# Kernel optimization log

Hardware: AMD Instinct MI355X
Metric: run time of the kernel (lower is better)

The kernel has to match this reference:

```python
import jax, jax.numpy as jnp
import numpy as np

EPSILON = 1e-05


def setup_inputs() -> dict:
    key = jax.random.key(0)
    X = jax.random.normal(key, (4, 2048, 3), dtype=jnp.float32)
    K = jnp.ones((), dtype=jnp.float32)
    B = jnp.zeros((), dtype=jnp.float32)
    return {"X": X, "K": K, "B": B}


def reference(X, K, B):
    # X: [batch, N, D]
    delta_X = X[:, :, None, :] - X[:, None, :, :]          # [b, N, N, D]
    sq = jnp.sum(delta_X * delta_X, axis=-1, keepdims=True)  # [b, N, N, 1]
    # safe sqrt: distance is 0 on the diagonal; avoid nan-producing grad paths
    distance = jnp.sqrt(jnp.where(sq == 0, 1.0, sq))
    distance = jnp.where(sq == 0, 0.0, distance)
    direction = delta_X / (distance + EPSILON)
    force = (K * (distance - B)) * direction               # [b, N, N, D]
    aggregated_force = jnp.sum(force, axis=-2)             # [b, N, D]
    return X + aggregated_force
```

## Files before the change

kernel.cpp:

```cpp
#include <hip/hip_runtime.h>

#define NPTS 2048

__global__ __launch_bounds__(256, 4) void spring_kernel(
    const float* __restrict__ X,
    const float* __restrict__ Kp,
    const float* __restrict__ Bp,
    float* __restrict__ out)
{
    __shared__ __align__(16) float xs[NPTS];
    __shared__ __align__(16) float ys[NPTS];
    __shared__ __align__(16) float zs[NPTS];

    const int tid    = threadIdx.x;
    const int b      = blockIdx.x >> 8;
    const int i_base = (blockIdx.x & 255) << 3;
    const float* Xb  = X + b * (NPTS * 3);

    const float K  = Kp[0];
    const float KB = K * Bp[0];

    {
        const float4* Xb4 = (const float4*)Xb;
        float4* xs4w = (float4*)xs;
        float4* ys4w = (float4*)ys;
        float4* zs4w = (float4*)zs;
        #pragma unroll
        for (int g0 = 0; g0 < NPTS / 4; g0 += 256) {
            const int g = g0 + tid;
            float4 f0 = Xb4[3 * g + 0];
            float4 f1 = Xb4[3 * g + 1];
            float4 f2 = Xb4[3 * g + 2];
            xs4w[g] = make_float4(f0.x, f0.w, f1.z, f2.y);
            ys4w[g] = make_float4(f0.y, f1.x, f1.w, f2.z);
            zs4w[g] = make_float4(f0.z, f1.y, f2.x, f2.w);
        }
    }
    __syncthreads();

    const int wv   = tid >> 6;
    const int lane = tid & 63;
    const int i0   = i_base + wv * 2;

    const float xi0 = xs[i0],     yi0 = ys[i0],     zi0 = zs[i0];
    const float xi1 = xs[i0 + 1], yi1 = ys[i0 + 1], zi1 = zs[i0 + 1];

    float ax0 = 0.f, ay0 = 0.f, az0 = 0.f;
    float ax1 = 0.f, ay1 = 0.f, az1 = 0.f;

    const float4* xs4 = (const float4*)xs;
    const float4* ys4 = (const float4*)ys;
    const float4* zs4 = (const float4*)zs;

    #pragma unroll 4
    for (int t = 0; t < NPTS / 4 / 64; ++t) {
        const int idx = (t << 6) + lane;
        float4 jx = xs4[idx];
        float4 jy = ys4[idx];
        float4 jz = zs4[idx];
        const float jxa[4] = {jx.x, jx.y, jx.z, jx.w};
        const float jya[4] = {jy.x, jy.y, jy.z, jy.w};
        const float jza[4] = {jz.x, jz.y, jz.z, jz.w};

        #pragma unroll
        for (int c = 0; c < 4; ++c) {
            {
                float dx = xi0 - jxa[c];
                float dy = yi0 - jya[c];
                float dz = zi0 - jza[c];
                float sq = fmaf(dx, dx, fmaf(dy, dy, fmaf(dz, dz, 1e-30f)));
                float r  = __builtin_amdgcn_rsqf(sq);
                float s  = fmaf(-KB, r, K);
                ax0 = fmaf(dx, s, ax0);
                ay0 = fmaf(dy, s, ay0);
                az0 = fmaf(dz, s, az0);
            }
            {
                float dx = xi1 - jxa[c];
                float dy = yi1 - jya[c];
                float dz = zi1 - jza[c];
                float sq = fmaf(dx, dx, fmaf(dy, dy, fmaf(dz, dz, 1e-30f)));
                float r  = __builtin_amdgcn_rsqf(sq);
                float s  = fmaf(-KB, r, K);
                ax1 = fmaf(dx, s, ax1);
                ay1 = fmaf(dy, s, ay1);
                az1 = fmaf(dz, s, az1);
            }
        }
    }

    #pragma unroll
    for (int d = 32; d > 0; d >>= 1) {
        ax0 += __shfl_down(ax0, d, 64);
        ay0 += __shfl_down(ay0, d, 64);
        az0 += __shfl_down(az0, d, 64);
        ax1 += __shfl_down(ax1, d, 64);
        ay1 += __shfl_down(ay1, d, 64);
        az1 += __shfl_down(az1, d, 64);
    }

    if (lane == 0) {
        float* o = out + (b * NPTS + i0) * 3;
        o[0] = xi0 + ax0;
        o[1] = yi0 + ay0;
        o[2] = zi0 + az0;
        o[3] = xi1 + ax1;
        o[4] = yi1 + ay1;
        o[5] = zi1 + az1;
    }
}

extern "C" void kernel_launch(void* const* d_in, const int* in_sizes, int n_in,
                              void* d_out, int out_size, void* d_ws, size_t ws_size,
                              hipStream_t stream) {
    const float* X  = (const float*)d_in[0];
    const float* Kp = (const float*)d_in[1];
    const float* Bp = (const float*)d_in[2];
    float* out = (float*)d_out;

    dim3 grid(4 * (NPTS / 8));
    dim3 block(256);
    spring_kernel<<<grid, block, 0, stream>>>(X, Kp, Bp, out);
}
```

Measured before the change: 63.27 us.

## Use 512-thread blocks with one row per wave instead of two

Doubles the block size to 8 waves and assigns one target point per wave rather than two, simplifying staging to a single load iteration. This increases waves available for latency hiding. It gives up reuse of each shared-memory j-load across two rows, doubling LDS reads per interaction, and adds reduction work per row.

```diff
diff --git a/kernel.cpp b/kernel.cpp
--- a/kernel.cpp
+++ b/kernel.cpp
@@ -2,7 +2,7 @@
 
 #define NPTS 2048
 
-__global__ __launch_bounds__(256, 4) void spring_kernel(
+__global__ __launch_bounds__(512, 8) void spring_kernel(
     const float* __restrict__ X,
     const float* __restrict__ Kp,
     const float* __restrict__ Bp,
@@ -25,34 +25,29 @@
         float4* xs4w = (float4*)xs;
         float4* ys4w = (float4*)ys;
         float4* zs4w = (float4*)zs;
-        #pragma unroll
-        for (int g0 = 0; g0 < NPTS / 4; g0 += 256) {
-            const int g = g0 + tid;
-            float4 f0 = Xb4[3 * g + 0];
-            float4 f1 = Xb4[3 * g + 1];
-            float4 f2 = Xb4[3 * g + 2];
-            xs4w[g] = make_float4(f0.x, f0.w, f1.z, f2.y);
-            ys4w[g] = make_float4(f0.y, f1.x, f1.w, f2.z);
-            zs4w[g] = make_float4(f0.z, f1.y, f2.x, f2.w);
-        }
+        const int g = tid;
+        float4 f0 = Xb4[3 * g + 0];
+        float4 f1 = Xb4[3 * g + 1];
+        float4 f2 = Xb4[3 * g + 2];
+        xs4w[g] = make_float4(f0.x, f0.w, f1.z, f2.y);
+        ys4w[g] = make_float4(f0.y, f1.x, f1.w, f2.z);
+        zs4w[g] = make_float4(f0.z, f1.y, f2.x, f2.w);
     }
     __syncthreads();
 
     const int wv   = tid >> 6;
     const int lane = tid & 63;
-    const int i0   = i_base + wv * 2;
+    const int i    = i_base + wv;
 
-    const float xi0 = xs[i0],     yi0 = ys[i0],     zi0 = zs[i0];
-    const float xi1 = xs[i0 + 1], yi1 = ys[i0 + 1], zi1 = zs[i0 + 1];
+    const float xi = xs[i], yi = ys[i], zi = zs[i];
 
-    float ax0 = 0.f, ay0 = 0.f, az0 = 0.f;
-    float ax1 = 0.f, ay1 = 0.f, az1 = 0.f;
+    float ax = 0.f, ay = 0.f, az = 0.f;
 
     const float4* xs4 = (const float4*)xs;
     const float4* ys4 = (const float4*)ys;
     const float4* zs4 = (const float4*)zs;
 
-    #pragma unroll 4
+    #pragma unroll 2
     for (int t = 0; t < NPTS / 4 / 64; ++t) {
         const int idx = (t << 6) + lane;
         float4 jx = xs4[idx];
@@ -64,49 +59,30 @@
 
         #pragma unroll
         for (int c = 0; c < 4; ++c) {
-            {
-                float dx = xi0 - jxa[c];
-                float dy = yi0 - jya[c];
-                float dz = zi0 - jza[c];
-                float sq = fmaf(dx, dx, fmaf(dy, dy, fmaf(dz, dz, 1e-30f)));
-                float r  = __builtin_amdgcn_rsqf(sq);
-                float s  = fmaf(-KB, r, K);
-                ax0 = fmaf(dx, s, ax0);
-                ay0 = fmaf(dy, s, ay0);
-                az0 = fmaf(dz, s, az0);
-            }
-            {
-                float dx = xi1 - jxa[c];
-                float dy = yi1 - jya[c];
-                float dz = zi1 - jza[c];
-                float sq = fmaf(dx, dx, fmaf(dy, dy, fmaf(dz, dz, 1e-30f)));
-                float r  = __builtin_amdgcn_rsqf(sq);
-                float s  = fmaf(-KB, r, K);
-                ax1 = fmaf(dx, s, ax1);
-                ay1 = fmaf(dy, s, ay1);
-                az1 = fmaf(dz, s, az1);
-            }
+            float dx = xi - jxa[c];
+            float dy = yi - jya[c];
+            float dz = zi - jza[c];
+            float sq = fmaf(dx, dx, fmaf(dy, dy, fmaf(dz, dz, 1e-30f)));
+            float r  = __builtin_amdgcn_rsqf(sq);
+            float s  = fmaf(-KB, r, K);
+            ax = fmaf(dx, s, ax);
+            ay = fmaf(dy, s, ay);
+            az = fmaf(dz, s, az);
         }
     }
 
     #pragma unroll
     for (int d = 32; d > 0; d >>= 1) {
-        ax0 += __shfl_down(ax0, d, 64);
-        ay0 += __shfl_down(ay0, d, 64);
-        az0 += __shfl_down(az0, d, 64);
-        ax1 += __shfl_down(ax1, d, 64);
-        ay1 += __shfl_down(ay1, d, 64);
-        az1 += __shfl_down(az1, d, 64);
+        ax += __shfl_down(ax, d, 64);
+        ay += __shfl_down(ay, d, 64);
+        az += __shfl_down(az, d, 64);
     }
 
     if (lane == 0) {
-        float* o = out + (b * NPTS + i0) * 3;
-        o[0] = xi0 + ax0;
-        o[1] = yi0 + ay0;
-        o[2] = zi0 + az0;
-        o[3] = xi1 + ax1;
-        o[4] = yi1 + ay1;
-        o[5] = zi1 + az1;
+        float* o = out + (b * NPTS + i) * 3;
+        o[0] = xi + ax;
+        o[1] = yi + ay;
+        o[2] = zi + az;
     }
 }
 
@@ -119,6 +95,6 @@
     float* out = (float*)d_out;
 
     dim3 grid(4 * (NPTS / 8));
-    dim3 block(256);
+    dim3 block(512);
     spring_kernel<<<grid, block, 0, stream>>>(X, Kp, Bp, out);
 }
```

Result: no change. 63.09 us (-0.3%).
